# Optimization experiments

Hardware: AMD Instinct MI355X
Metric: run time of the kernel (lower is better)

## Reference

```python
import jax, jax.numpy as jnp
import numpy as np

D_MODEL = 512
N_PAIRS = D_MODEL // 2
B, T = 8, 4096


def setup_inputs() -> dict:
    key = jax.random.key(0)
    ks = jax.random.split(key, 7)
    scale = 1.0 / np.sqrt(D_MODEL)
    return {
        "x_seq": jax.random.normal(ks[0], (B, T, D_MODEL), dtype=jnp.float32),
        "W_angle": jax.random.uniform(ks[1], (D_MODEL, N_PAIRS), jnp.float32, -scale, scale),
        "b_angle": jnp.zeros((N_PAIRS,), jnp.float32),
        "W_decay": jax.random.uniform(ks[2], (D_MODEL, 1), jnp.float32, -scale, scale),
        "b_decay": jnp.full((1,), 1.4, jnp.float32),
        "W_input": jax.random.uniform(ks[3], (D_MODEL, D_MODEL), jnp.float32, -scale, scale),
        "b_input": jax.random.uniform(ks[4], (D_MODEL,), jnp.float32, -scale, scale),
    }


def _givens_ssm(x_seq, W_angle, b_angle, W_decay, b_decay, W_input, b_input):
    Bb, Tt, D = x_seq.shape
    P = D // 2
    angles = jnp.einsum("btd,dp->btp", x_seq, W_angle) + b_angle          # [B,T,P]
    decays = jax.nn.sigmoid(jnp.einsum("btd,dk->btk", x_seq, W_decay) + b_decay)[..., 0]  # [B,T]
    inj = jnp.einsum("btd,de->bte", x_seq, W_input) + b_input              # [B,T,D]
    inj = inj.reshape(Bb, Tt, P, 2)

    # scan over time: h_t = decay_t * Rot(angles_t) h_{t-1} + inj_t, pairwise 2x2 rotations
    def step(h, inp):
        a, d, u = inp  # a:[B,P], d:[B], u:[B,P,2]
        c, s = jnp.cos(a), jnp.sin(a)
        he = c * h[..., 0] - s * h[..., 1]
        ho = s * h[..., 0] + c * h[..., 1]
        h_new = d[:, None, None] * jnp.stack([he, ho], axis=-1) + u
        return h_new, h_new

    h0 = jnp.zeros((Bb, P, 2), x_seq.dtype)
    xs = (jnp.swapaxes(angles, 0, 1), jnp.swapaxes(decays, 0, 1), jnp.swapaxes(inj, 0, 1))
    _, states = jax.lax.scan(step, h0, xs)  # [T,B,P,2]
    return jnp.swapaxes(states, 0, 1).reshape(Bb, Tt, D)


def reference(x_seq, W_angle, b_angle, W_decay, b_decay, W_input, b_input):
    return _givens_ssm(x_seq, W_angle, b_angle, W_decay, b_decay, W_input, b_input)
```

## Files before the change

### kernel.cpp

```cpp
#include <hip/hip_runtime.h>
#include <math.h>

typedef _Float16 half_t;
typedef __attribute__((ext_vector_type(8))) _Float16 half8;
typedef __attribute__((ext_vector_type(4))) _Float16 half4;
typedef __attribute__((ext_vector_type(4))) float floatx4;

#define BATCH   8
#define SEQ     4096
#define DM      512
#define NP      256
#define M_TOT   32768
#define NTOT    768
#define CHUNKS  128
#define CHUNK_LEN 32

__device__ __forceinline__ void async_load16(const void* g, void* l) {
    __builtin_amdgcn_global_load_lds((const __attribute__((address_space(1))) void*)g,
                                     (__attribute__((address_space(3))) void*)l,
                                     16, 0, 0);
}

__global__ __launch_bounds__(256) void decay_convert(const float* __restrict__ X,
                                                     const float* __restrict__ Wd,
                                                     const float* __restrict__ bd,
                                                     float* __restrict__ dec,
                                                     half_t* __restrict__ Xh) {
    const int wave = threadIdx.x >> 6;
    const int lane = threadIdx.x & 63;
    const int row  = blockIdx.x * 4 + wave;
    const float4* xr = (const float4*)(X + (size_t)row * DM);
    const float4* wd = (const float4*)Wd;
    float sum = 0.0f;
#pragma unroll
    for (int i = 0; i < 2; ++i) {
        const int c = lane + i * 64;
        float4 v = xr[c];
        float4 w = wd[c];
        sum += v.x * w.x + v.y * w.y + v.z * w.z + v.w * w.w;
        half4 h = {(half_t)v.x, (half_t)v.y, (half_t)v.z, (half_t)v.w};
        *(half4*)(Xh + (size_t)row * DM + c * 4) = h;
    }
#pragma unroll
    for (int off = 32; off > 0; off >>= 1) sum += __shfl_down(sum, off, 64);
    if (lane == 0) {
        float z = sum + bd[0];
        dec[row] = 1.0f / (1.0f + __expf(-z));
    }
}

__global__ __launch_bounds__(256) void wcat_transpose(const float* __restrict__ Wi,
                                                      const float* __restrict__ Wa,
                                                      half_t* __restrict__ Wt) {
    const int idx = blockIdx.x * 256 + threadIdx.x;
    const int n = idx >> 9;
    const int k = idx & 511;
    float v = (n < DM) ? Wi[(size_t)k * DM + n] : Wa[(size_t)k * NP + (n - DM)];
    Wt[idx] = (half_t)v;
}

__global__ __launch_bounds__(256) void gemm_fused(const half_t* __restrict__ Xh,
                                                  const half_t* __restrict__ Wt,
                                                  const float* __restrict__ bi,
                                                  const float* __restrict__ ba,
                                                  float* __restrict__ out,
                                                  half_t* __restrict__ angles) {
    __shared__ __align__(16) char As[8192];
    __shared__ __align__(16) char Bs[8192];

    const int bm   = blockIdx.x;
    const int bn   = blockIdx.y;
    const int tid  = threadIdx.x;
    const int wave = tid >> 6;
    const int lane = tid & 63;
    const int quad = lane >> 4;
    const int l16  = lane & 15;
    const int wrow = wave >> 1;
    const int wcol = wave & 1;

    floatx4 acc[4][4];
#pragma unroll
    for (int i = 0; i < 4; ++i)
#pragma unroll
        for (int j = 0; j < 4; ++j) acc[i][j] = (floatx4){0.f, 0.f, 0.f, 0.f};

    const int s0 = wave * 128 + lane;
    const int s1 = s0 + 64;
    const int r0 = s0 >> 2, kql0 = (s0 & 3) ^ ((r0 >> 1) & 3);
    const int r1 = s1 >> 2, kql1 = (s1 & 3) ^ ((r1 >> 1) & 3);
    const half_t* gA0 = Xh + (size_t)(bm * 128 + r0) * DM + kql0 * 8;
    const half_t* gA1 = Xh + (size_t)(bm * 128 + r1) * DM + kql1 * 8;
    const half_t* gB0 = Wt + (size_t)(bn * 128 + r0) * DM + kql0 * 8;
    const half_t* gB1 = Wt + (size_t)(bn * 128 + r1) * DM + kql1 * 8;
    char* lA0 = As + wave * 2048;
    char* lA1 = As + wave * 2048 + 1024;
    char* lB0 = Bs + wave * 2048;
    char* lB1 = Bs + wave * 2048 + 1024;

    for (int k0 = 0; k0 < DM; k0 += 32) {
        async_load16(gA0 + k0, lA0);
        async_load16(gA1 + k0, lA1);
        async_load16(gB0 + k0, lB0);
        async_load16(gB1 + k0, lB1);
        __syncthreads();

        half8 af[4], bf[4];
#pragma unroll
        for (int mt = 0; mt < 4; ++mt) {
            const int r = wrow * 64 + mt * 16 + l16;
            af[mt] = *(const half8*)(As + r * 64 + ((quad ^ ((r >> 1) & 3)) << 4));
        }
#pragma unroll
        for (int nt = 0; nt < 4; ++nt) {
            const int r = wcol * 64 + nt * 16 + l16;
            bf[nt] = *(const half8*)(Bs + r * 64 + ((quad ^ ((r >> 1) & 3)) << 4));
        }
#pragma unroll
        for (int mt = 0; mt < 4; ++mt)
#pragma unroll
            for (int nt = 0; nt < 4; ++nt)
                acc[mt][nt] = __builtin_amdgcn_mfma_f32_16x16x32_f16(af[mt], bf[nt],
                                                                     acc[mt][nt], 0, 0, 0);
        __syncthreads();
    }

    const int colbase = bn * 128 + wcol * 64;
#pragma unroll
    for (int nt = 0; nt < 4; ++nt) {
        const int col = colbase + nt * 16 + l16;
        const bool is_inj = col < DM;
        const float bias = is_inj ? bi[col] : ba[col - DM];
#pragma unroll
        for (int mt = 0; mt < 4; ++mt) {
            const int rowb = bm * 128 + wrow * 64 + mt * 16 + quad * 4;
#pragma unroll
            for (int r = 0; r < 4; ++r) {
                const float v = acc[mt][nt][r] + bias;
                const int row = rowb + r;
                if (is_inj) out[(size_t)row * DM + col] = v;
                else        angles[(size_t)row * NP + (col - DM)] = (half_t)v;
            }
        }
    }
}

__global__ __launch_bounds__(256) void scan_phase1(const half_t* __restrict__ angles,
                                                   const float* __restrict__ decays,
                                                   float* __restrict__ out,
                                                   float* __restrict__ thetaC,
                                                   float2* __restrict__ hend,
                                                   float* __restrict__ Dprod) {
    const int b = blockIdx.x / CHUNKS;
    const int c = blockIdx.x % CHUNKS;
    const int p = threadIdx.x;
    const int t0 = c * CHUNK_LEN;
    float2* out2 = (float2*)out;

    float h0 = 0.0f, h1 = 0.0f, th = 0.0f, dc = 1.0f;
#pragma unroll 4
    for (int i = 0; i < CHUNK_LEN; ++i) {
        const int t = t0 + i;
        const size_t idx = (size_t)(b * SEQ + t) * NP + p;
        float a = (float)angles[idx];
        float d = decays[b * SEQ + t];
        float2 u = out2[idx];
        float s, cc;
        __sincosf(a, &s, &cc);
        float he = cc * h0 - s * h1;
        float ho = s * h0 + cc * h1;
        h0 = fmaf(d, he, u.x);
        h1 = fmaf(d, ho, u.y);
        out2[idx] = make_float2(h0, h1);
        th += a;
        dc *= d;
    }
    const size_t cidx = (size_t)(b * CHUNKS + c) * NP + p;
    thetaC[cidx] = th;
    hend[cidx]   = make_float2(h0, h1);
    if (p == 0) Dprod[b * CHUNKS + c] = dc;
}

__global__ __launch_bounds__(256) void scan_chunks(const float* __restrict__ thetaC,
                                                   const float2* __restrict__ hend,
                                                   const float* __restrict__ Dprod,
                                                   float2* __restrict__ hentry) {
    const int b = blockIdx.x;
    const int p = threadIdx.x;
    float h0 = 0.0f, h1 = 0.0f;
    for (int c = 0; c < CHUNKS; ++c) {
        const size_t cidx = (size_t)(b * CHUNKS + c) * NP + p;
        hentry[cidx] = make_float2(h0, h1);
        float th = thetaC[cidx];
        float D  = Dprod[b * CHUNKS + c];
        float2 he = hend[cidx];
        float s, cc;
        __sincosf(th, &s, &cc);
        float n0 = fmaf(D, cc * h0 - s * h1, he.x);
        float n1 = fmaf(D, s * h0 + cc * h1, he.y);
        h0 = n0;
        h1 = n1;
    }
}

__global__ __launch_bounds__(256) void scan_fixup(const half_t* __restrict__ angles,
                                                  const float* __restrict__ decays,
                                                  const float2* __restrict__ hentry,
                                                  float* __restrict__ out) {
    const int b = blockIdx.x / CHUNKS;
    const int c = blockIdx.x % CHUNKS;
    if (c == 0) return;
    const int p = threadIdx.x;
    const int t0 = c * CHUNK_LEN;
    float2* out2 = (float2*)out;

    float2 v = hentry[(size_t)(b * CHUNKS + c) * NP + p];
#pragma unroll 4
    for (int i = 0; i < CHUNK_LEN; ++i) {
        const int t = t0 + i;
        const size_t idx = (size_t)(b * SEQ + t) * NP + p;
        float a = (float)angles[idx];
        float d = decays[b * SEQ + t];
        float s, cc;
        __sincosf(a, &s, &cc);
        float n0 = d * (cc * v.x - s * v.y);
        float n1 = d * (s * v.x + cc * v.y);
        v = make_float2(n0, n1);
        float2 o = out2[idx];
        o.x += v.x;
        o.y += v.y;
        out2[idx] = o;
    }
}

extern "C" void kernel_launch(void* const* d_in, const int* in_sizes, int n_in,
                              void* d_out, int out_size, void* d_ws, size_t ws_size,
                              hipStream_t stream) {
    const float* x  = (const float*)d_in[0];
    const float* Wa = (const float*)d_in[1];
    const float* ba = (const float*)d_in[2];
    const float* Wd = (const float*)d_in[3];
    const float* bd = (const float*)d_in[4];
    const float* Wi = (const float*)d_in[5];
    const float* bi = (const float*)d_in[6];
    float* out = (float*)d_out;

    char* ws = (char*)d_ws;
    half_t* x_h     = (half_t*)(ws);
    float*  thetaC  = (float*)(ws);
    float2* hend    = (float2*)(ws + 1048576);
    float*  Dprod   = (float*)(ws + 3145728);
    float2* hentry  = (float2*)(ws + 3149824);
    half_t* angles  = (half_t*)(ws + 33554432);
    float*  decays  = (float*)(ws + 50331648);
    half_t* Wcat_t  = (half_t*)(ws + 50462720);

    decay_convert<<<M_TOT / 4, 256, 0, stream>>>(x, Wd, bd, decays, x_h);
    wcat_transpose<<<(NTOT * DM) / 256, 256, 0, stream>>>(Wi, Wa, Wcat_t);
    gemm_fused<<<dim3(M_TOT / 128, NTOT / 128), 256, 0, stream>>>(x_h, Wcat_t, bi, ba, out, angles);

    scan_phase1<<<BATCH * CHUNKS, 256, 0, stream>>>(angles, decays, out, thetaC, hend, Dprod);
    scan_chunks<<<BATCH, 256, 0, stream>>>(thetaC, hend, Dprod, hentry);
    scan_fixup<<<BATCH * CHUNKS, 256, 0, stream>>>(angles, decays, hentry, out);
}
```

Before: 232.4 us.

## Restructure scan to summary-then-final pass, vectorize loads, double-K GEMM stage

The chunked scan changes from write-then-fixup to a summary-only first pass that no longer writes out, followed by a final pass that recomputes the full recurrence from the chunk entry state and writes out once. This removes one read-modify-write of the output buffer. Scan threads now handle two pairs each with float4/half2 vector accesses. The GEMM loads two 32-wide K slices per barrier pair, halving the number of syncs, and the convert kernel uses wider 16-byte half8 stores. In exchange, the final pass now also computes chunk 0, and LDS use per GEMM block doubles.

```diff
diff --git a/kernel.cpp b/kernel.cpp
--- a/kernel.cpp
+++ b/kernel.cpp
@@ -4,6 +4,7 @@
 typedef _Float16 half_t;
 typedef __attribute__((ext_vector_type(8))) _Float16 half8;
 typedef __attribute__((ext_vector_type(4))) _Float16 half4;
+typedef __attribute__((ext_vector_type(2))) _Float16 half2v;
 typedef __attribute__((ext_vector_type(4))) float floatx4;
 
 #define BATCH   8
@@ -31,16 +32,13 @@
     const int row  = blockIdx.x * 4 + wave;
     const float4* xr = (const float4*)(X + (size_t)row * DM);
     const float4* wd = (const float4*)Wd;
-    float sum = 0.0f;
-#pragma unroll
-    for (int i = 0; i < 2; ++i) {
-        const int c = lane + i * 64;
-        float4 v = xr[c];
-        float4 w = wd[c];
-        sum += v.x * w.x + v.y * w.y + v.z * w.z + v.w * w.w;
-        half4 h = {(half_t)v.x, (half_t)v.y, (half_t)v.z, (half_t)v.w};
-        *(half4*)(Xh + (size_t)row * DM + c * 4) = h;
-    }
+    float4 v0 = xr[2 * lane], v1 = xr[2 * lane + 1];
+    float4 w0 = wd[2 * lane], w1 = wd[2 * lane + 1];
+    float sum = v0.x * w0.x + v0.y * w0.y + v0.z * w0.z + v0.w * w0.w
+              + v1.x * w1.x + v1.y * w1.y + v1.z * w1.z + v1.w * w1.w;
+    half8 h = {(half_t)v0.x, (half_t)v0.y, (half_t)v0.z, (half_t)v0.w,
+               (half_t)v1.x, (half_t)v1.y, (half_t)v1.z, (half_t)v1.w};
+    *(half8*)(Xh + (size_t)row * DM + lane * 8) = h;
 #pragma unroll
     for (int off = 32; off > 0; off >>= 1) sum += __shfl_down(sum, off, 64);
     if (lane == 0) {
@@ -65,8 +63,8 @@
                                                   const float* __restrict__ ba,
                                                   float* __restrict__ out,
                                                   half_t* __restrict__ angles) {
-    __shared__ __align__(16) char As[8192];
-    __shared__ __align__(16) char Bs[8192];
+    __shared__ __align__(16) char As[2][8192];
+    __shared__ __align__(16) char Bs[2][8192];
 
     const int bm   = blockIdx.x;
     const int bn   = blockIdx.y;
@@ -92,35 +90,38 @@
     const half_t* gA1 = Xh + (size_t)(bm * 128 + r1) * DM + kql1 * 8;
     const half_t* gB0 = Wt + (size_t)(bn * 128 + r0) * DM + kql0 * 8;
     const half_t* gB1 = Wt + (size_t)(bn * 128 + r1) * DM + kql1 * 8;
-    char* lA0 = As + wave * 2048;
-    char* lA1 = As + wave * 2048 + 1024;
-    char* lB0 = Bs + wave * 2048;
-    char* lB1 = Bs + wave * 2048 + 1024;
-
-    for (int k0 = 0; k0 < DM; k0 += 32) {
-        async_load16(gA0 + k0, lA0);
-        async_load16(gA1 + k0, lA1);
-        async_load16(gB0 + k0, lB0);
-        async_load16(gB1 + k0, lB1);
+
+    for (int k0 = 0; k0 < DM; k0 += 64) {
+#pragma unroll
+        for (int kb = 0; kb < 2; ++kb) {
+            const int ko = k0 + kb * 32;
+            async_load16(gA0 + ko, As[kb] + wave * 2048);
+            async_load16(gA1 + ko, As[kb] + wave * 2048 + 1024);
+            async_load16(gB0 + ko, Bs[kb] + wave * 2048);
+            async_load16(gB1 + ko, Bs[kb] + wave * 2048 + 1024);
+        }
         __syncthreads();
 
-        half8 af[4], bf[4];
-#pragma unroll
-        for (int mt = 0; mt < 4; ++mt) {
-            const int r = wrow * 64 + mt * 16 + l16;
-            af[mt] = *(const half8*)(As + r * 64 + ((quad ^ ((r >> 1) & 3)) << 4));
+#pragma unroll
+        for (int kb = 0; kb < 2; ++kb) {
+            half8 af[4], bf[4];
+#pragma unroll
+            for (int mt = 0; mt < 4; ++mt) {
+                const int r = wrow * 64 + mt * 16 + l16;
+                af[mt] = *(const half8*)(As[kb] + r * 64 + ((quad ^ ((r >> 1) & 3)) << 4));
+            }
+#pragma unroll
+            for (int nt = 0; nt < 4; ++nt) {
+                const int r = wcol * 64 + nt * 16 + l16;
+                bf[nt] = *(const half8*)(Bs[kb] + r * 64 + ((quad ^ ((r >> 1) & 3)) << 4));
+            }
+#pragma unroll
+            for (int mt = 0; mt < 4; ++mt)
+#pragma unroll
+                for (int nt = 0; nt < 4; ++nt)
+                    acc[mt][nt] = __builtin_amdgcn_mfma_f32_16x16x32_f16(af[mt], bf[nt],
+                                                                         acc[mt][nt], 0, 0, 0);
         }
-#pragma unroll
-        for (int nt = 0; nt < 4; ++nt) {
-            const int r = wcol * 64 + nt * 16 + l16;
-            bf[nt] = *(const half8*)(Bs + r * 64 + ((quad ^ ((r >> 1) & 3)) << 4));
-        }
-#pragma unroll
-        for (int mt = 0; mt < 4; ++mt)
-#pragma unroll
-            for (int nt = 0; nt < 4; ++nt)
-                acc[mt][nt] = __builtin_amdgcn_mfma_f32_16x16x32_f16(af[mt], bf[nt],
-                                                                     acc[mt][nt], 0, 0, 0);
         __syncthreads();
     }
 
@@ -144,91 +145,100 @@
     }
 }
 
-__global__ __launch_bounds__(256) void scan_phase1(const half_t* __restrict__ angles,
-                                                   const float* __restrict__ decays,
-                                                   float* __restrict__ out,
-                                                   float* __restrict__ thetaC,
-                                                   float2* __restrict__ hend,
-                                                   float* __restrict__ Dprod) {
-    const int b = blockIdx.x / CHUNKS;
-    const int c = blockIdx.x % CHUNKS;
-    const int p = threadIdx.x;
-    const int t0 = c * CHUNK_LEN;
-    float2* out2 = (float2*)out;
-
-    float h0 = 0.0f, h1 = 0.0f, th = 0.0f, dc = 1.0f;
+__global__ __launch_bounds__(256) void scan_sum1(const half_t* __restrict__ angles,
+                                                 const float* __restrict__ decays,
+                                                 const float* __restrict__ inj,
+                                                 float* __restrict__ thetaC,
+                                                 float4* __restrict__ hend,
+                                                 float* __restrict__ Dprod) {
+    const int b    = blockIdx.x >> 6;
+    const int sub  = threadIdx.x >> 7;
+    const int th   = threadIdx.x & 127;
+    const int c    = (blockIdx.x & 63) * 2 + sub;
+    const int p0   = th * 2;
+    const int t0   = c * CHUNK_LEN;
+    const float4* inj4 = (const float4*)inj;
+
+    float h0a = 0, h1a = 0, h0b = 0, h1b = 0, tha = 0, thb = 0, dc = 1.0f;
 #pragma unroll 4
     for (int i = 0; i < CHUNK_LEN; ++i) {
         const int t = t0 + i;
-        const size_t idx = (size_t)(b * SEQ + t) * NP + p;
-        float a = (float)angles[idx];
+        const size_t base = (size_t)(b * SEQ + t) * NP + p0;
+        half2v av = *(const half2v*)(angles + base);
+        float4 u = inj4[base >> 1];
         float d = decays[b * SEQ + t];
-        float2 u = out2[idx];
-        float s, cc;
-        __sincosf(a, &s, &cc);
-        float he = cc * h0 - s * h1;
-        float ho = s * h0 + cc * h1;
-        h0 = fmaf(d, he, u.x);
-        h1 = fmaf(d, ho, u.y);
-        out2[idx] = make_float2(h0, h1);
-        th += a;
-        dc *= d;
-    }
-    const size_t cidx = (size_t)(b * CHUNKS + c) * NP + p;
-    thetaC[cidx] = th;
-    hend[cidx]   = make_float2(h0, h1);
-    if (p == 0) Dprod[b * CHUNKS + c] = dc;
-}
-
-__global__ __launch_bounds__(256) void scan_chunks(const float* __restrict__ thetaC,
-                                                   const float2* __restrict__ hend,
+        float a0 = (float)av[0], a1 = (float)av[1];
+        float s0, c0, s1, c1;
+        __sincosf(a0, &s0, &c0);
+        __sincosf(a1, &s1, &c1);
+        float n0a = fmaf(d, c0 * h0a - s0 * h1a, u.x);
+        float n1a = fmaf(d, s0 * h0a + c0 * h1a, u.y);
+        float n0b = fmaf(d, c1 * h0b - s1 * h1b, u.z);
+        float n1b = fmaf(d, s1 * h0b + c1 * h1b, u.w);
+        h0a = n0a; h1a = n1a; h0b = n0b; h1b = n1b;
+        tha += a0; thb += a1; dc *= d;
+    }
+    const size_t cbase = (size_t)(b * CHUNKS + c) * NP + p0;
+    *(float2*)(thetaC + cbase) = make_float2(tha, thb);
+    hend[cbase >> 1] = make_float4(h0a, h1a, h0b, h1b);
+    if (th == 0) Dprod[b * CHUNKS + c] = dc;
+}
+
+__global__ __launch_bounds__(128) void scan_chunks(const float* __restrict__ thetaC,
+                                                   const float4* __restrict__ hend,
                                                    const float* __restrict__ Dprod,
-                                                   float2* __restrict__ hentry) {
-    const int b = blockIdx.x;
-    const int p = threadIdx.x;
-    float h0 = 0.0f, h1 = 0.0f;
+                                                   float4* __restrict__ hentry) {
+    const int b  = blockIdx.x;
+    const int p0 = threadIdx.x * 2;
+    float h0a = 0, h1a = 0, h0b = 0, h1b = 0;
     for (int c = 0; c < CHUNKS; ++c) {
-        const size_t cidx = (size_t)(b * CHUNKS + c) * NP + p;
-        hentry[cidx] = make_float2(h0, h1);
-        float th = thetaC[cidx];
-        float D  = Dprod[b * CHUNKS + c];
-        float2 he = hend[cidx];
-        float s, cc;
-        __sincosf(th, &s, &cc);
-        float n0 = fmaf(D, cc * h0 - s * h1, he.x);
-        float n1 = fmaf(D, s * h0 + cc * h1, he.y);
-        h0 = n0;
-        h1 = n1;
-    }
-}
-
-__global__ __launch_bounds__(256) void scan_fixup(const half_t* __restrict__ angles,
+        const size_t cbase = (size_t)(b * CHUNKS + c) * NP + p0;
+        hentry[cbase >> 1] = make_float4(h0a, h1a, h0b, h1b);
+        float2 th2 = *(const float2*)(thetaC + cbase);
+        float D = Dprod[b * CHUNKS + c];
+        float4 he = hend[cbase >> 1];
+        float s0, c0, s1, c1;
+        __sincosf(th2.x, &s0, &c0);
+        __sincosf(th2.y, &s1, &c1);
+        float n0a = fmaf(D, c0 * h0a - s0 * h1a, he.x);
+        float n1a = fmaf(D, s0 * h0a + c0 * h1a, he.y);
+        float n0b = fmaf(D, c1 * h0b - s1 * h1b, he.z);
+        float n1b = fmaf(D, s1 * h0b + c1 * h1b, he.w);
+        h0a = n0a; h1a = n1a; h0b = n0b; h1b = n1b;
+    }
+}
+
+__global__ __launch_bounds__(256) void scan_final(const half_t* __restrict__ angles,
                                                   const float* __restrict__ decays,
-                                                  const float2* __restrict__ hentry,
+                                                  const float4* __restrict__ hentry,
                                                   float* __restrict__ out) {
-    const int b = blockIdx.x / CHUNKS;
-    const int c = blockIdx.x % CHUNKS;
-    if (c == 0) return;
-    const int p = threadIdx.x;
-    const int t0 = c * CHUNK_LEN;
-    float2* out2 = (float2*)out;
-
-    float2 v = hentry[(size_t)(b * CHUNKS + c) * NP + p];
+    const int b    = blockIdx.x >> 6;
+    const int sub  = threadIdx.x >> 7;
+    const int th   = threadIdx.x & 127;
+    const int c    = (blockIdx.x & 63) * 2 + sub;
+    const int p0   = th * 2;
+    const int t0   = c * CHUNK_LEN;
+    float4* out4 = (float4*)out;
+
+    float4 v = hentry[((size_t)(b * CHUNKS + c) * NP + p0) >> 1];
+    float h0a = v.x, h1a = v.y, h0b = v.z, h1b = v.w;
 #pragma unroll 4
     for (int i = 0; i < CHUNK_LEN; ++i) {
         const int t = t0 + i;
-        const size_t idx = (size_t)(b * SEQ + t) * NP + p;
-        float a = (float)angles[idx];
+        const size_t base = (size_t)(b * SEQ + t) * NP + p0;
+        half2v av = *(const half2v*)(angles + base);
+        float4 u = out4[base >> 1];
         float d = decays[b * SEQ + t];
-        float s, cc;
-        __sincosf(a, &s, &cc);
-        float n0 = d * (cc * v.x - s * v.y);
-        float n1 = d * (s * v.x + cc * v.y);
-        v = make_float2(n0, n1);
-        float2 o = out2[idx];
-        o.x += v.x;
-        o.y += v.y;
-        out2[idx] = o;
+        float a0 = (float)av[0], a1 = (float)av[1];
+        float s0, c0, s1, c1;
+        __sincosf(a0, &s0, &c0);
+        __sincosf(a1, &s1, &c1);
+        float n0a = fmaf(d, c0 * h0a - s0 * h1a, u.x);
+        float n1a = fmaf(d, s0 * h0a + c0 * h1a, u.y);
+        float n0b = fmaf(d, c1 * h0b - s1 * h1b, u.z);
+        float n1b = fmaf(d, s1 * h0b + c1 * h1b, u.w);
+        h0a = n0a; h1a = n1a; h0b = n0b; h1b = n1b;
+        out4[base >> 1] = make_float4(h0a, h1a, h0b, h1b);
     }
 }
 
@@ -247,9 +257,9 @@
     char* ws = (char*)d_ws;
     half_t* x_h     = (half_t*)(ws);
     float*  thetaC  = (float*)(ws);
-    float2* hend    = (float2*)(ws + 1048576);
+    float4* hend    = (float4*)(ws + 1048576);
     float*  Dprod   = (float*)(ws + 3145728);
-    float2* hentry  = (float2*)(ws + 3149824);
+    float4* hentry  = (float4*)(ws + 3149824);
     half_t* angles  = (half_t*)(ws + 33554432);
     float*  decays  = (float*)(ws + 50331648);
     half_t* Wcat_t  = (half_t*)(ws + 50462720);
@@ -258,7 +268,7 @@
     wcat_transpose<<<(NTOT * DM) / 256, 256, 0, stream>>>(Wi, Wa, Wcat_t);
     gemm_fused<<<dim3(M_TOT / 128, NTOT / 128), 256, 0, stream>>>(x_h, Wcat_t, bi, ba, out, angles);
 
-    scan_phase1<<<BATCH * CHUNKS, 256, 0, stream>>>(angles, decays, out, thetaC, hend, Dprod);
-    scan_chunks<<<BATCH, 256, 0, stream>>>(thetaC, hend, Dprod, hentry);
-    scan_fixup<<<BATCH * CHUNKS, 256, 0, stream>>>(angles, decays, hentry, out);
-}
+    scan_sum1<<<BATCH * CHUNKS / 2, 256, 0, stream>>>(angles, decays, out, thetaC, hend, Dprod);
+    scan_chunks<<<BATCH, 128, 0, stream>>>(thetaC, hend, Dprod, hentry);
+    scan_final<<<BATCH * CHUNKS / 2, 256, 0, stream>>>(angles, decays, hentry, out);
+}
```

Measured after the change: 236.2 us. About the same (+1.6%).
